# Kernel optimization log

Hardware: AMD Instinct MI355X
Metric: run time of the kernel (lower is better)

Reference implementation:

```python
import jax, jax.numpy as jnp
import numpy as np

B, T, H, D = 4, 4096, 1024, 4  # batch, seq_len, hidden_size, max_depth


def setup_inputs() -> dict:
    key = jax.random.key(0)
    ks = jax.random.split(key, 8)
    s = 1.0 / np.sqrt(H)
    x = jax.random.normal(ks[0], (B, T, H), dtype=jnp.float32)
    state = jax.random.normal(ks[1], (B, D, H), dtype=jnp.float32)
    # time_decay_multi initialized as in the torch module: row d = 0.9**(d+1)
    time_decay_multi = jnp.broadcast_to(
        (0.9 ** jnp.arange(1, D + 1, dtype=jnp.float32))[:, None], (D, H)
    ).astype(jnp.float32)
    Wl = jax.random.uniform(ks[2], (D, H), jnp.float32, -s, s)   # level_selector weight [out=D, in=H]
    bl = jax.random.uniform(ks[3], (D,), jnp.float32, -s, s)
    Wv = jax.random.uniform(ks[4], (H, H), jnp.float32, -s, s)
    Wk = jax.random.uniform(ks[5], (H, H), jnp.float32, -s, s)
    Wr = jax.random.uniform(ks[6], (H, H), jnp.float32, -s, s)
    Wo = jax.random.uniform(ks[7], (H, H), jnp.float32, -s, s)
    return {"x": x, "state": state, "time_decay_multi": time_decay_multi,
            "Wl": Wl, "bl": bl, "Wv": Wv, "Wk": Wk, "Wr": Wr, "Wo": Wo}


def reference(x, state, time_decay_multi, Wl, bl, Wv, Wk, Wr, Wo):
    # Projections (torch Linear: y = x @ W.T)
    v = jnp.einsum('bth,oh->bto', x, Wv)
    k = jnp.einsum('bth,oh->bto', x, Wk)
    r = jax.nn.sigmoid(jnp.einsum('bth,oh->bto', x, Wr))
    level_weights = jax.nn.softmax(jnp.einsum('bth,dh->btd', x, Wl) + bl, axis=-1)  # [B,T,D]

    decay = jnp.exp(-jnp.exp(time_decay_multi))        # [D,H]
    decayed_state0 = state * decay[None]               # [B,D,H] (original state is never updated in the loop)
    kv = k * v                                         # [B,T,H]

    # per-step state for depth d is decayed_state0[b,d] + kv[b,t]; weighted sum over depths:
    weighted = (jnp.einsum('btd,bdh->bth', level_weights, decayed_state0)
                + jnp.sum(level_weights, axis=-1, keepdims=True) * kv)  # [B,T,H]
    o = r * weighted
    output = jnp.einsum('bth,oh->bto', o, Wo)

    # new_state after the loop keeps only the LAST timestep contribution
    new_state = decayed_state0 + kv[:, -1][:, None, :]  # [B,D,H]
    return output, new_state
```

## Files before the change

### kernel.cpp

```cpp
#include <hip/hip_runtime.h>

#define B_ 4
#define T_ 4096
#define H_ 1024
#define D_ 4
#define M_ (B_ * T_)
#define OUT_MAIN (M_ * H_)

#define WS_BUF  0UL
#define WS_WK   33554432UL
#define WS_LGW  41943040UL
#define WS_DEC  42205184UL

typedef __bf16 bf16x8 __attribute__((ext_vector_type(8)));
typedef unsigned short u16x4 __attribute__((ext_vector_type(4)));
typedef float f32x4 __attribute__((ext_vector_type(4)));

__device__ __forceinline__ float b2f(unsigned short u) {
    union { unsigned int i; float f; } c;
    c.i = ((unsigned int)u) << 16;
    return c.f;
}
__device__ __forceinline__ unsigned short f2b(float f) {
    union { float f; unsigned int i; } c;
    c.f = f;
    unsigned int x = c.i;
    unsigned int r = (x + 0x7FFFu + ((x >> 16) & 1u)) >> 16;
    return (unsigned short)r;
}

#define BAR()  asm volatile("s_barrier" ::: "memory")
#define GLLDS(gsrc, ldst)                                                     \
    __builtin_amdgcn_global_load_lds(                                         \
        (const __attribute__((address_space(1))) unsigned int*)(gsrc),        \
        (__attribute__((address_space(3))) unsigned int*)(ldst), 16, 0, 0)

__global__ __launch_bounds__(256) void cvtw_k(
    const float* __restrict__ s0, const float* __restrict__ s1,
    const float* __restrict__ s2, const float* __restrict__ s3,
    unsigned short* __restrict__ d)
{
    const int w = blockIdx.y;
    const float* s = (w == 0) ? s0 : (w == 1) ? s1 : (w == 2) ? s2 : s3;
    const int i = blockIdx.x * 256 + threadIdx.x;
    const f32x4 v = ((const f32x4*)s)[i];
    u16x4 o;
    o[0] = f2b(v[0]); o[1] = f2b(v[1]); o[2] = f2b(v[2]); o[3] = f2b(v[3]);
    ((u16x4*)(d + (size_t)w * (H_ * H_)))[i] = o;
}

__global__ __launch_bounds__(256) void logcvt_k(
    const float* __restrict__ X, const float* __restrict__ Wl,
    const float* __restrict__ bl, float* __restrict__ lgw,
    unsigned short* __restrict__ xb)
{
    const int wid  = threadIdx.x >> 6;
    const int lane = threadIdx.x & 63;
    const int row  = blockIdx.x * 4 + wid;
    const float* xp = X + (size_t)row * H_;
    unsigned short* xo = xb + (size_t)row * H_;

    float acc[D_] = {0.f, 0.f, 0.f, 0.f};
    for (int h = lane * 4; h < H_; h += 256) {
        const f32x4 xv = *(const f32x4*)(xp + h);
        u16x4 xc;
        xc[0] = f2b(xv[0]); xc[1] = f2b(xv[1]);
        xc[2] = f2b(xv[2]); xc[3] = f2b(xv[3]);
        *(u16x4*)(xo + h) = xc;
#pragma unroll
        for (int d = 0; d < D_; ++d) {
            const f32x4 wv = *(const f32x4*)(Wl + d * H_ + h);
            acc[d] += xv[0] * wv[0] + xv[1] * wv[1] + xv[2] * wv[2] + xv[3] * wv[3];
        }
    }
#pragma unroll
    for (int off = 32; off; off >>= 1)
#pragma unroll
        for (int d = 0; d < D_; ++d) acc[d] += __shfl_xor(acc[d], off, 64);

    if (lane == 0) {
        float l[D_];
#pragma unroll
        for (int d = 0; d < D_; ++d) l[d] = acc[d] + bl[d];
        const float mx = fmaxf(fmaxf(l[0], l[1]), fmaxf(l[2], l[3]));
        float e[D_], s = 0.f;
#pragma unroll
        for (int d = 0; d < D_; ++d) { e[d] = __expf(l[d] - mx); s += e[d]; }
        const float inv = 1.0f / s;
        f32x4 o;
#pragma unroll
        for (int d = 0; d < D_; ++d) o[d] = e[d] * inv;
        *(f32x4*)(lgw + (size_t)row * 4) = o;
    }
}

__global__ void decstate_k(const float* __restrict__ state,
                           const float* __restrict__ tdm,
                           float* __restrict__ dec)
{
    const int i = blockIdx.x * blockDim.x + threadIdx.x;
    if (i >= B_ * D_ * H_) return;
    const int dh = i & (D_ * H_ - 1);
    dec[i] = state[i] * __expf(-__expf(tdm[dh]));
}

__global__ __launch_bounds__(256) void newstate_k(
    const float* __restrict__ X, const float* __restrict__ Wk,
    const float* __restrict__ Wv, const float* __restrict__ dec,
    float* __restrict__ out2)
{
    const int wid  = threadIdx.x >> 6;
    const int lane = threadIdx.x & 63;
    const int row  = blockIdx.x * 4 + wid;
    const int b    = row >> 10;
    const int h    = row & (H_ - 1);
    const float* xp = X + ((size_t)(b * T_ + (T_ - 1))) * H_;

    float ak = 0.f, av = 0.f;
    for (int j = lane * 4; j < H_; j += 256) {
        const f32x4 xv = *(const f32x4*)(xp + j);
        const f32x4 wk = *(const f32x4*)(Wk + (size_t)h * H_ + j);
        const f32x4 wv = *(const f32x4*)(Wv + (size_t)h * H_ + j);
        ak += xv[0]*wk[0] + xv[1]*wk[1] + xv[2]*wk[2] + xv[3]*wk[3];
        av += xv[0]*wv[0] + xv[1]*wv[1] + xv[2]*wv[2] + xv[3]*wv[3];
    }
#pragma unroll
    for (int off = 32; off; off >>= 1) {
        ak += __shfl_xor(ak, off, 64);
        av += __shfl_xor(av, off, 64);
    }
    if (lane == 0) {
        const float kv = ak * av;
#pragma unroll
        for (int d = 0; d < D_; ++d)
            out2[(size_t)(b * D_ + d) * H_ + h] = dec[(b * D_ + d) * H_ + h] + kv;
    }
}

__global__ __launch_bounds__(512, 2) void gemm_kvr(
    const unsigned short* __restrict__ A,
    const unsigned short* __restrict__ Wk,
    const unsigned short* __restrict__ Wv,
    const unsigned short* __restrict__ Wr,
    unsigned short* __restrict__ Co,
    const float* __restrict__ lgw,
    const float* __restrict__ dec)
{
    __shared__ __align__(16) unsigned short As [2 * 8192];
    __shared__ __align__(16) unsigned short Bks[2 * 8192];
    __shared__ __align__(16) unsigned short Bvs[2 * 8192];
    __shared__ __align__(16) unsigned short Brs[2 * 8192];

    const int tid  = threadIdx.x;
    const int wid  = tid >> 6;
    const int lane = tid & 63;
    const int l15  = lane & 15;
    const int q    = lane >> 4;
    const int wrow = wid >> 2;
    const int wcol = wid & 3;
    const int bcol = blockIdx.x * 128;
    const int brow = blockIdx.y * 128;

    const int g0row = tid >> 3, g0cg = (tid & 7) ^ (g0row & 7);
    const int g1row = 64 + g0row, g1cg = (tid & 7) ^ (g1row & 7);
    const int offA0 = (brow + g0row) * 1024 + g0cg * 8;
    const int offA1 = (brow + g1row) * 1024 + g1cg * 8;
    const int offB0 = (bcol + g0row) * 1024 + g0cg * 8;
    const int offB1 = (bcol + g1row) * 1024 + g1cg * 8;
    const int dst0 = tid * 8;
    const int dst1 = 4096 + tid * 8;

    int gx[2];
#pragma unroll
    for (int ks = 0; ks < 2; ++ks) gx[ks] = ((ks * 4 + q) ^ (l15 & 7)) * 8;
    int aB[4], bB[2];
#pragma unroll
    for (int mi = 0; mi < 4; ++mi) aB[mi] = (wrow * 64 + mi * 16 + l15) * 64;
#pragma unroll
    for (int ni = 0; ni < 2; ++ni) bB[ni] = (wcol * 32 + ni * 16 + l15) * 64;

    f32x4 accK[4][2], accV[4][2], accR[4][2];
#pragma unroll
    for (int i = 0; i < 4; ++i)
#pragma unroll
        for (int j = 0; j < 2; ++j) {
            accK[i][j] = (f32x4){0.f, 0.f, 0.f, 0.f};
            accV[i][j] = (f32x4){0.f, 0.f, 0.f, 0.f};
            accR[i][j] = (f32x4){0.f, 0.f, 0.f, 0.f};
        }

#define SG_A(bo, tau)  do { GLLDS(A  + offA0 + (tau) * 64, As  + (bo) + dst0); \
                            GLLDS(A  + offA1 + (tau) * 64, As  + (bo) + dst1); } while (0)
#define SG_BK(bo, tau) do { GLLDS(Wk + offB0 + (tau) * 64, Bks + (bo) + dst0); \
                            GLLDS(Wk + offB1 + (tau) * 64, Bks + (bo) + dst1); } while (0)
#define SG_BV(bo, tau) do { GLLDS(Wv + offB0 + (tau) * 64, Bvs + (bo) + dst0); \
                            GLLDS(Wv + offB1 + (tau) * 64, Bvs + (bo) + dst1); } while (0)
#define SG_BR(bo, tau) do { GLLDS(Wr + offB0 + (tau) * 64, Brs + (bo) + dst0); \
                            GLLDS(Wr + offB1 + (tau) * 64, Brs + (bo) + dst1); } while (0)
#define RD_AALL(CUR)                                                          \
    _Pragma("unroll") for (int mi = 0; mi < 4; ++mi)                          \
    _Pragma("unroll") for (int ks = 0; ks < 2; ++ks)                          \
        aR[mi][ks] = *(const bf16x8*)&As[(CUR) + aB[mi] + gx[ks]];
#define RD_B(ARR, CUR)                                                        \
    _Pragma("unroll") for (int nj = 0; nj < 2; ++nj)                          \
    _Pragma("unroll") for (int ks = 0; ks < 2; ++ks)                          \
        bR[nj][ks] = *(const bf16x8*)&ARR[(CUR) + bB[nj] + gx[ks]];
#define MFMA16(ACC)                                                           \
    __builtin_amdgcn_s_setprio(1);                                            \
    _Pragma("unroll") for (int mi = 0; mi < 4; ++mi)                          \
    _Pragma("unroll") for (int nj = 0; nj < 2; ++nj)                          \
    _Pragma("unroll") for (int ks = 0; ks < 2; ++ks)                          \
        ACC[mi][nj] = __builtin_amdgcn_mfma_f32_16x16x32_bf16(                \
            aR[mi][ks], bR[nj][ks], ACC[mi][nj], 0, 0, 0);                    \
    __builtin_amdgcn_s_setprio(0);

    SG_A(0, 0); SG_BK(0, 0); SG_BV(0, 0); SG_BR(0, 0);
    asm volatile("s_waitcnt vmcnt(4)" ::: "memory");
    BAR();

#pragma unroll 1
    for (int t = 0; t < 15; ++t) {
        const int cur = (t & 1) << 13;
        const int nxt = cur ^ 8192;
        bf16x8 aR[4][2], bR[2][2];

        RD_AALL(cur); RD_B(Bks, cur);
        SG_A(nxt, t + 1); SG_BK(nxt, t + 1);
        BAR(); MFMA16(accK);
        asm volatile("s_waitcnt vmcnt(6)" ::: "memory");
        BAR();

        RD_B(Bvs, cur);
        SG_BV(nxt, t + 1);
        BAR(); MFMA16(accV);
        asm volatile("s_waitcnt vmcnt(6)" ::: "memory");
        BAR();

        RD_B(Brs, cur);
        SG_BR(nxt, t + 1);
        BAR(); MFMA16(accR);
        asm volatile("s_waitcnt vmcnt(4)" ::: "memory");
        BAR();
    }
    {
        const int cur = 8192;
        bf16x8 aR[4][2], bR[2][2];
        RD_AALL(cur); RD_B(Bks, cur);
        BAR(); MFMA16(accK);
        asm volatile("s_waitcnt vmcnt(2)" ::: "memory");
        BAR();
        RD_B(Bvs, cur);
        BAR(); MFMA16(accV);
        asm volatile("s_waitcnt vmcnt(0)" ::: "memory");
        BAR();
        RD_B(Brs, cur);
        MFMA16(accR);
    }
#undef SG_A
#undef SG_BK
#undef SG_BV
#undef SG_BR
#undef RD_AALL
#undef RD_B
#undef MFMA16

    const int orow0 = brow + wrow * 64;
    const int ocol0 = bcol + wcol * 32;
    const int rbase = q * 4;
    const int b = brow >> 12;
    float dcol[2][4];
#pragma unroll
    for (int ni = 0; ni < 2; ++ni)
#pragma unroll
        for (int d = 0; d < 4; ++d)
            dcol[ni][d] = dec[b * (D_ * H_) + d * H_ + (ocol0 + ni * 16 + l15)];
#pragma unroll
    for (int mi = 0; mi < 4; ++mi)
#pragma unroll
        for (int j = 0; j < 4; ++j) {
            const int r = orow0 + mi * 16 + rbase + j;
            const f32x4 lw = *(const f32x4*)(lgw + (size_t)r * 4);
            const float wsum = lw[0] + lw[1] + lw[2] + lw[3];
#pragma unroll
            for (int ni = 0; ni < 2; ++ni) {
                const size_t idx = (size_t)r * 1024 + (ocol0 + ni * 16 + l15);
                const float kvf = b2f(f2b(accV[mi][ni][j] * b2f(f2b(accK[mi][ni][j]))));
                const float rv  = 1.0f / (1.0f + __expf(-accR[mi][ni][j]));
                const float w   = lw[0] * dcol[ni][0] + lw[1] * dcol[ni][1]
                                + lw[2] * dcol[ni][2] + lw[3] * dcol[ni][3]
                                + wsum * kvf;
                Co[idx] = f2b(rv * w);
            }
        }
}

__global__ __launch_bounds__(512, 2) void gemm_o(
    const unsigned short* __restrict__ A,
    const unsigned short* __restrict__ Wt,
    float* __restrict__ outf)
{
    __shared__ __align__(16) unsigned short As[2 * 256 * 64];
    __shared__ __align__(16) unsigned short Bs[2 * 256 * 64];

    const int tid  = threadIdx.x;
    const int wid  = tid >> 6;
    const int lane = tid & 63;
    const int l15  = lane & 15;
    const int l7   = lane & 7;
    const int wrow = wid >> 2;
    const int wcol = wid & 3;
    const int brow = blockIdx.x * 256;
    const int bcol = blockIdx.y * 256;

    int offA[4], offB[4], dst[4];
#pragma unroll
    for (int i = 0; i < 4; ++i) {
        const int G   = i * 512 + tid;
        const int row = G >> 3;
        const int cg  = (G & 7) ^ (row & 7);
        offA[i] = (brow + row) * 1024 + cg * 8;
        offB[i] = (bcol + row) * 1024 + cg * 8;
        dst[i]  = G * 8;
    }

    int aB[8], bB[4], gx[2];
#pragma unroll
    for (int ks = 0; ks < 2; ++ks) gx[ks] = ((ks * 4 + (lane >> 4)) ^ l7) * 8;
#pragma unroll
    for (int mi = 0; mi < 8; ++mi) aB[mi] = (wrow * 128 + mi * 16 + l15) * 64;
#pragma unroll
    for (int ni = 0; ni < 4; ++ni) bB[ni] = (wcol * 64 + ni * 16 + l15) * 64;

    f32x4 acc[8][4];
#pragma unroll
    for (int i = 0; i < 8; ++i)
#pragma unroll
        for (int j = 0; j < 4; ++j)
            acc[i][j] = (f32x4){0.f, 0.f, 0.f, 0.f};

#pragma unroll
    for (int i = 0; i < 4; ++i) {
        GLLDS(A  + offA[i], As + dst[i]);
        GLLDS(Wt + offB[i], Bs + dst[i]);
    }
    asm volatile("s_waitcnt vmcnt(0)" ::: "memory");
    BAR();

#pragma unroll 1
    for (int t = 0; t < 16; ++t) {
        const int cur = (t & 1) * 16384;
        const int nxt = 16384 - cur;
        const int kk  = (t + 1) * 64;
        const bool st = (t < 15);
        bf16x8 aR[4][2], bR[4][2];

#pragma unroll
        for (int mi = 0; mi < 4; ++mi)
#pragma unroll
            for (int ks = 0; ks < 2; ++ks)
                aR[mi][ks] = *(const bf16x8*)&As[cur + aB[mi] + gx[ks]];
#pragma unroll
        for (int ni = 0; ni < 2; ++ni)
#pragma unroll
            for (int ks = 0; ks < 2; ++ks)
                bR[ni][ks] = *(const bf16x8*)&Bs[cur + bB[ni] + gx[ks]];
        if (st) {
            GLLDS(A  + offA[0] + kk, As + nxt + dst[0]);
            GLLDS(A  + offA[1] + kk, As + nxt + dst[1]);
            GLLDS(Wt + offB[0] + kk, Bs + nxt + dst[0]);
        }
        BAR();
        __builtin_amdgcn_s_setprio(1);
#pragma unroll
        for (int mi = 0; mi < 4; ++mi)
#pragma unroll
            for (int ni = 0; ni < 2; ++ni)
#pragma unroll
                for (int ks = 0; ks < 2; ++ks)
                    acc[mi][ni] = __builtin_amdgcn_mfma_f32_16x16x32_bf16(
                        aR[mi][ks], bR[ni][ks], acc[mi][ni], 0, 0, 0);
        __builtin_amdgcn_s_setprio(0);
        BAR();

#pragma unroll
        for (int ni = 2; ni < 4; ++ni)
#pragma unroll
            for (int ks = 0; ks < 2; ++ks)
                bR[ni][ks] = *(const bf16x8*)&Bs[cur + bB[ni] + gx[ks]];
        if (st) {
            GLLDS(A  + offA[2] + kk, As + nxt + dst[2]);
            GLLDS(A  + offA[3] + kk, As + nxt + dst[3]);
            GLLDS(Wt + offB[1] + kk, Bs + nxt + dst[1]);
        }
        BAR();
        __builtin_amdgcn_s_setprio(1);
#pragma unroll
        for (int mi = 0; mi < 4; ++mi)
#pragma unroll
            for (int ni = 2; ni < 4; ++ni)
#pragma unroll
                for (int ks = 0; ks < 2; ++ks)
                    acc[mi][ni] = __builtin_amdgcn_mfma_f32_16x16x32_bf16(
                        aR[mi][ks], bR[ni][ks], acc[mi][ni], 0, 0, 0);
        __builtin_amdgcn_s_setprio(0);
        BAR();

#pragma unroll
        for (int mi = 0; mi < 4; ++mi)
#pragma unroll
            for (int ks = 0; ks < 2; ++ks)
                aR[mi][ks] = *(const bf16x8*)&As[cur + aB[4 + mi] + gx[ks]];
        if (st) {
            GLLDS(Wt + offB[2] + kk, Bs + nxt + dst[2]);
            GLLDS(Wt + offB[3] + kk, Bs + nxt + dst[3]);
        }
        BAR();
        __builtin_amdgcn_s_setprio(1);
#pragma unroll
        for (int mi = 0; mi < 4; ++mi)
#pragma unroll
            for (int ni = 2; ni < 4; ++ni)
#pragma unroll
                for (int ks = 0; ks < 2; ++ks)
                    acc[4 + mi][ni] = __builtin_amdgcn_mfma_f32_16x16x32_bf16(
                        aR[mi][ks], bR[ni][ks], acc[4 + mi][ni], 0, 0, 0);
        __builtin_amdgcn_s_setprio(0);
        BAR();

        __builtin_amdgcn_s_setprio(1);
#pragma unroll
        for (int mi = 0; mi < 4; ++mi)
#pragma unroll
            for (int ni = 0; ni < 2; ++ni)
#pragma unroll
                for (int ks = 0; ks < 2; ++ks)
                    acc[4 + mi][ni] = __builtin_amdgcn_mfma_f32_16x16x32_bf16(
                        aR[mi][ks], bR[ni][ks], acc[4 + mi][ni], 0, 0, 0);
        __builtin_amdgcn_s_setprio(0);
        asm volatile("s_waitcnt vmcnt(0)" ::: "memory");
        BAR();
    }

    const int orow0 = brow + wrow * 128;
    const int ocol0 = bcol + wcol * 64;
    const int rbase = (lane >> 4) * 4;
#pragma unroll
    for (int mi = 0; mi < 8; ++mi)
#pragma unroll
        for (int j = 0; j < 4; ++j) {
            const size_t r = (size_t)(orow0 + mi * 16 + rbase + j);
#pragma unroll
            for (int ni = 0; ni < 4; ++ni)
                outf[r * 1024 + (ocol0 + ni * 16 + l15)] = acc[mi][ni][j];
        }
}

extern "C" void kernel_launch(void* const* d_in, const int* in_sizes, int n_in,
                              void* d_out, int out_size, void* d_ws, size_t ws_size,
                              hipStream_t stream)
{
    const float* x   = (const float*)d_in[0];
    const float* st  = (const float*)d_in[1];
    const float* tdm = (const float*)d_in[2];
    const float* Wl  = (const float*)d_in[3];
    const float* bl  = (const float*)d_in[4];
    const float* Wv  = (const float*)d_in[5];
    const float* Wk  = (const float*)d_in[6];
    const float* Wr  = (const float*)d_in[7];
    const float* Wo  = (const float*)d_in[8];
    float* out = (float*)d_out;

    char* ws = (char*)d_ws;
    unsigned short* buf  = (unsigned short*)(ws + WS_BUF);
    unsigned short* wk_b = (unsigned short*)(ws + WS_WK);
    unsigned short* wv_b = wk_b + 1 * (H_ * H_);
    unsigned short* wr_b = wk_b + 2 * (H_ * H_);
    unsigned short* wo_b = wk_b + 3 * (H_ * H_);
    float* lgw = (float*)(ws + WS_LGW);
    float* dec = (float*)(ws + WS_DEC);

    unsigned short* xb = (unsigned short*)out;

    decstate_k<<<(B_ * D_ * H_ + 255) / 256, 256, 0, stream>>>(st, tdm, dec);
    logcvt_k<<<M_ / 4, 256, 0, stream>>>(x, Wl, bl, lgw, xb);
    newstate_k<<<(B_ * H_) / 4, 256, 0, stream>>>(x, Wk, Wv, dec, out + OUT_MAIN);
    cvtw_k<<<dim3(1024, 4), 256, 0, stream>>>(Wk, Wv, Wr, Wo, wk_b);

    gemm_kvr<<<dim3(H_ / 128, M_ / 128), 512, 0, stream>>>(
        xb, wk_b, wv_b, wr_b, buf, lgw, dec);

    gemm_o<<<dim3(M_ / 256, H_ / 256), 512, 0, stream>>>(buf, wo_b, out);
}
```

Before: 177.0 us.

## Retile output GEMM to 256x128 blocks with deeper A-prefetch pipeline

The output projection GEMM moves from 256x256 tiles (8 waves, each 128x64) to 256x128 tiles (8 waves, each 64x64). The grid doubles along the column axis. The A tile is now prefetched two k-steps ahead, using partial vmcnt waits instead of a full drain every iteration. This aims to cut per-wave register pressure, raise block count and occupancy, and hide global load latency better. The cost is that A tiles are reloaded twice as often across column blocks.

```diff
diff --git a/kernel.cpp b/kernel.cpp
--- a/kernel.cpp
+++ b/kernel.cpp
@@ -294,158 +294,122 @@
         }
 }
 
-__global__ __launch_bounds__(512, 2) void gemm_o(
+__global__ __launch_bounds__(512, 2) void gemm_o2(
     const unsigned short* __restrict__ A,
     const unsigned short* __restrict__ Wt,
     float* __restrict__ outf)
 {
-    __shared__ __align__(16) unsigned short As[2 * 256 * 64];
-    __shared__ __align__(16) unsigned short Bs[2 * 256 * 64];
+    __shared__ __align__(16) unsigned short As[2 * 16384];
+    __shared__ __align__(16) unsigned short Bs[2 * 8192];
 
     const int tid  = threadIdx.x;
     const int wid  = tid >> 6;
     const int lane = tid & 63;
     const int l15  = lane & 15;
-    const int l7   = lane & 7;
-    const int wrow = wid >> 2;
-    const int wcol = wid & 3;
+    const int q    = lane >> 4;
+    const int wrow = wid >> 1;
+    const int wcol = wid & 1;
     const int brow = blockIdx.x * 256;
-    const int bcol = blockIdx.y * 256;
-
-    int offA[4], offB[4], dst[4];
+    const int bcol = blockIdx.y * 128;
+
+    int offA[4], dstA[4];
 #pragma unroll
     for (int i = 0; i < 4; ++i) {
         const int G   = i * 512 + tid;
         const int row = G >> 3;
         const int cg  = (G & 7) ^ (row & 7);
         offA[i] = (brow + row) * 1024 + cg * 8;
-        offB[i] = (bcol + row) * 1024 + cg * 8;
-        dst[i]  = G * 8;
-    }
-
-    int aB[8], bB[4], gx[2];
-#pragma unroll
-    for (int ks = 0; ks < 2; ++ks) gx[ks] = ((ks * 4 + (lane >> 4)) ^ l7) * 8;
-#pragma unroll
-    for (int mi = 0; mi < 8; ++mi) aB[mi] = (wrow * 128 + mi * 16 + l15) * 64;
+        dstA[i] = G * 8;
+    }
+    int offB[2], dstB[2];
+#pragma unroll
+    for (int j = 0; j < 2; ++j) {
+        const int G   = j * 512 + tid;
+        const int row = G >> 3;
+        const int cg  = (G & 7) ^ (row & 7);
+        offB[j] = (bcol + row) * 1024 + cg * 8;
+        dstB[j] = G * 8;
+    }
+
+    int gx[2];
+#pragma unroll
+    for (int ks = 0; ks < 2; ++ks) gx[ks] = ((ks * 4 + q) ^ (l15 & 7)) * 8;
+    int aB[4], bB[4];
+#pragma unroll
+    for (int mi = 0; mi < 4; ++mi) aB[mi] = (wrow * 64 + mi * 16 + l15) * 64;
 #pragma unroll
     for (int ni = 0; ni < 4; ++ni) bB[ni] = (wcol * 64 + ni * 16 + l15) * 64;
 
-    f32x4 acc[8][4];
-#pragma unroll
-    for (int i = 0; i < 8; ++i)
+    f32x4 acc[4][4];
+#pragma unroll
+    for (int i = 0; i < 4; ++i)
 #pragma unroll
         for (int j = 0; j < 4; ++j)
             acc[i][j] = (f32x4){0.f, 0.f, 0.f, 0.f};
 
-#pragma unroll
-    for (int i = 0; i < 4; ++i) {
-        GLLDS(A  + offA[i], As + dst[i]);
-        GLLDS(Wt + offB[i], Bs + dst[i]);
-    }
-    asm volatile("s_waitcnt vmcnt(0)" ::: "memory");
+#define SG_A(bo, tau)  do { GLLDS(A + offA[0] + (tau) * 64, As + (bo) + dstA[0]); \
+                            GLLDS(A + offA[1] + (tau) * 64, As + (bo) + dstA[1]); \
+                            GLLDS(A + offA[2] + (tau) * 64, As + (bo) + dstA[2]); \
+                            GLLDS(A + offA[3] + (tau) * 64, As + (bo) + dstA[3]); } while (0)
+#define SG_B(bo, tau)  do { GLLDS(Wt + offB[0] + (tau) * 64, Bs + (bo) + dstB[0]); \
+                            GLLDS(Wt + offB[1] + (tau) * 64, Bs + (bo) + dstB[1]); } while (0)
+#define RD_AALL(CUR)                                                          \
+    _Pragma("unroll") for (int mi = 0; mi < 4; ++mi)                          \
+    _Pragma("unroll") for (int ks = 0; ks < 2; ++ks)                          \
+        aR[mi][ks] = *(const bf16x8*)&As[(CUR) + aB[mi] + gx[ks]];
+#define RD_B2(CUR, N0)                                                        \
+    _Pragma("unroll") for (int nj = 0; nj < 2; ++nj)                          \
+    _Pragma("unroll") for (int ks = 0; ks < 2; ++ks)                          \
+        bR[nj][ks] = *(const bf16x8*)&Bs[(CUR) + bB[(N0) + nj] + gx[ks]];
+#define MFMA16(N0)                                                            \
+    __builtin_amdgcn_s_setprio(1);                                            \
+    _Pragma("unroll") for (int mi = 0; mi < 4; ++mi)                          \
+    _Pragma("unroll") for (int nj = 0; nj < 2; ++nj)                          \
+    _Pragma("unroll") for (int ks = 0; ks < 2; ++ks)                          \
+        acc[mi][(N0) + nj] = __builtin_amdgcn_mfma_f32_16x16x32_bf16(         \
+            aR[mi][ks], bR[nj][ks], acc[mi][(N0) + nj], 0, 0, 0);             \
+    __builtin_amdgcn_s_setprio(0);
+
+    SG_A(0, 0); SG_B(0, 0); SG_A(16384, 1);
+    asm volatile("s_waitcnt vmcnt(4)" ::: "memory");
     BAR();
 
 #pragma unroll 1
-    for (int t = 0; t < 16; ++t) {
-        const int cur = (t & 1) * 16384;
-        const int nxt = 16384 - cur;
-        const int kk  = (t + 1) * 64;
-        const bool st = (t < 15);
-        bf16x8 aR[4][2], bR[4][2];
-
-#pragma unroll
-        for (int mi = 0; mi < 4; ++mi)
-#pragma unroll
-            for (int ks = 0; ks < 2; ++ks)
-                aR[mi][ks] = *(const bf16x8*)&As[cur + aB[mi] + gx[ks]];
-#pragma unroll
-        for (int ni = 0; ni < 2; ++ni)
-#pragma unroll
-            for (int ks = 0; ks < 2; ++ks)
-                bR[ni][ks] = *(const bf16x8*)&Bs[cur + bB[ni] + gx[ks]];
-        if (st) {
-            GLLDS(A  + offA[0] + kk, As + nxt + dst[0]);
-            GLLDS(A  + offA[1] + kk, As + nxt + dst[1]);
-            GLLDS(Wt + offB[0] + kk, Bs + nxt + dst[0]);
-        }
-        BAR();
-        __builtin_amdgcn_s_setprio(1);
-#pragma unroll
-        for (int mi = 0; mi < 4; ++mi)
-#pragma unroll
-            for (int ni = 0; ni < 2; ++ni)
-#pragma unroll
-                for (int ks = 0; ks < 2; ++ks)
-                    acc[mi][ni] = __builtin_amdgcn_mfma_f32_16x16x32_bf16(
-                        aR[mi][ks], bR[ni][ks], acc[mi][ni], 0, 0, 0);
-        __builtin_amdgcn_s_setprio(0);
-        BAR();
-
-#pragma unroll
-        for (int ni = 2; ni < 4; ++ni)
-#pragma unroll
-            for (int ks = 0; ks < 2; ++ks)
-                bR[ni][ks] = *(const bf16x8*)&Bs[cur + bB[ni] + gx[ks]];
-        if (st) {
-            GLLDS(A  + offA[2] + kk, As + nxt + dst[2]);
-            GLLDS(A  + offA[3] + kk, As + nxt + dst[3]);
-            GLLDS(Wt + offB[1] + kk, Bs + nxt + dst[1]);
-        }
-        BAR();
-        __builtin_amdgcn_s_setprio(1);
-#pragma unroll
-        for (int mi = 0; mi < 4; ++mi)
-#pragma unroll
-            for (int ni = 2; ni < 4; ++ni)
-#pragma unroll
-                for (int ks = 0; ks < 2; ++ks)
-                    acc[mi][ni] = __builtin_amdgcn_mfma_f32_16x16x32_bf16(
-                        aR[mi][ks], bR[ni][ks], acc[mi][ni], 0, 0, 0);
-        __builtin_amdgcn_s_setprio(0);
-        BAR();
-
-#pragma unroll
-        for (int mi = 0; mi < 4; ++mi)
-#pragma unroll
-            for (int ks = 0; ks < 2; ++ks)
-                aR[mi][ks] = *(const bf16x8*)&As[cur + aB[4 + mi] + gx[ks]];
-        if (st) {
-            GLLDS(Wt + offB[2] + kk, Bs + nxt + dst[2]);
-            GLLDS(Wt + offB[3] + kk, Bs + nxt + dst[3]);
-        }
-        BAR();
-        __builtin_amdgcn_s_setprio(1);
-#pragma unroll
-        for (int mi = 0; mi < 4; ++mi)
-#pragma unroll
-            for (int ni = 2; ni < 4; ++ni)
-#pragma unroll
-                for (int ks = 0; ks < 2; ++ks)
-                    acc[4 + mi][ni] = __builtin_amdgcn_mfma_f32_16x16x32_bf16(
-                        aR[mi][ks], bR[ni][ks], acc[4 + mi][ni], 0, 0, 0);
-        __builtin_amdgcn_s_setprio(0);
-        BAR();
-
-        __builtin_amdgcn_s_setprio(1);
-#pragma unroll
-        for (int mi = 0; mi < 4; ++mi)
-#pragma unroll
-            for (int ni = 0; ni < 2; ++ni)
-#pragma unroll
-                for (int ks = 0; ks < 2; ++ks)
-                    acc[4 + mi][ni] = __builtin_amdgcn_mfma_f32_16x16x32_bf16(
-                        aR[mi][ks], bR[ni][ks], acc[4 + mi][ni], 0, 0, 0);
-        __builtin_amdgcn_s_setprio(0);
-        asm volatile("s_waitcnt vmcnt(0)" ::: "memory");
-        BAR();
-    }
-
-    const int orow0 = brow + wrow * 128;
+    for (int t = 0; t < 15; ++t) {
+        const int curA = (t & 1) << 14;
+        const int curB = (t & 1) << 13;
+        const int nxtB = curB ^ 8192;
+        bf16x8 aR[4][2], bR[2][2];
+
+        RD_AALL(curA); RD_B2(curB, 0);
+        SG_B(nxtB, t + 1);
+        BAR(); MFMA16(0); BAR();
+
+        RD_B2(curB, 2);
+        if (t < 14) SG_A(curA, t + 2);
+        BAR(); MFMA16(2);
+        if (t < 14) asm volatile("s_waitcnt vmcnt(4)" ::: "memory");
+        else        asm volatile("s_waitcnt vmcnt(0)" ::: "memory");
+        BAR();
+    }
+    {
+        const int curA = 16384, curB = 8192;
+        bf16x8 aR[4][2], bR[2][2];
+        RD_AALL(curA);
+        RD_B2(curB, 0); MFMA16(0);
+        RD_B2(curB, 2); MFMA16(2);
+    }
+#undef SG_A
+#undef SG_B
+#undef RD_AALL
+#undef RD_B2
+#undef MFMA16
+
+    const int orow0 = brow + wrow * 64;
     const int ocol0 = bcol + wcol * 64;
-    const int rbase = (lane >> 4) * 4;
-#pragma unroll
-    for (int mi = 0; mi < 8; ++mi)
+    const int rbase = q * 4;
+#pragma unroll
+    for (int mi = 0; mi < 4; ++mi)
 #pragma unroll
         for (int j = 0; j < 4; ++j) {
             const size_t r = (size_t)(orow0 + mi * 16 + rbase + j);
@@ -489,5 +453,5 @@
     gemm_kvr<<<dim3(H_ / 128, M_ / 128), 512, 0, stream>>>(
         xb, wk_b, wv_b, wr_b, buf, lgw, dec);
 
-    gemm_o<<<dim3(M_ / 256, H_ / 256), 512, 0, stream>>>(buf, wo_b, out);
-}
+    gemm_o2<<<dim3(M_ / 256, H_ / 128), 512, 0, stream>>>(buf, wo_b, out);
+}
```

New measurement: 191.3 us. 1.08x slower.
